# Kernel optimization log

Hardware: AMD Instinct MI355X
Metric: run time of the kernel (lower is better)

Reference implementation:

```python
import jax, jax.numpy as jnp
import numpy as np

N = 50000
E = 800000
DIN = 128
DH = [128, 128]
DOUT = 64


def setup_inputs() -> dict:
    key = jax.random.key(0)
    ks = jax.random.split(key, 12)

    def w(k, fan_in, fan_out):
        return jax.random.normal(k, (fan_in, fan_out), dtype=jnp.float32) / np.sqrt(fan_in)

    x = jax.random.normal(ks[0], (N, DIN), dtype=jnp.float32)
    edge_index = jax.random.randint(ks[1], (2, E), 0, N, dtype=jnp.int64)
    return {
        "x": x,
        "edge_index": edge_index,
        # SAGEConv layer 0: lin_l (aggregated neighbors, with bias), lin_r (root, no bias)
        "Wl0": w(ks[2], DIN, DH[0]), "Wr0": w(ks[3], DIN, DH[0]), "b0": jnp.zeros((DH[0],), jnp.float32),
        # SAGEConv layer 1
        "Wl1": w(ks[4], DH[0], DH[1]), "Wr1": w(ks[5], DH[0], DH[1]), "b1": jnp.zeros((DH[1],), jnp.float32),
        # final Linear
        "Wout": w(ks[6], DH[1], DOUT), "bout": jnp.zeros((DOUT,), jnp.float32),
    }


def sage_conv(h, src, dst, Wl, Wr, b):
    # mean-aggregate source features at destination nodes
    msg = h[src]                                                  # [E, d]
    agg = jax.ops.segment_sum(msg, dst, num_segments=N)           # [N, d]
    cnt = jax.ops.segment_sum(jnp.ones((src.shape[0],), h.dtype), dst, num_segments=N)
    agg = agg / jnp.maximum(cnt, 1.0)[:, None]
    return agg @ Wl + h @ Wr + b


def reference(x, edge_index, Wl0, Wr0, b0, Wl1, Wr1, b1, Wout, bout):
    src, dst = edge_index[0], edge_index[1]
    h = jax.nn.relu(sage_conv(x, src, dst, Wl0, Wr0, b0))
    # dropout: identity in eval mode
    h = jax.nn.relu(sage_conv(h, src, dst, Wl1, Wr1, b1))
    out = h @ Wout + bout                                         # [N, DOUT]
    return jax.nn.softmax(out, axis=1)
```

## Files before the change

kernel.cpp:

```cpp
#include <hip/hip_runtime.h>


#define CAP 64
#define NBK 256
#define EPB 2048
#define BCAP8 768
#define ASTR 136

typedef __attribute__((ext_vector_type(8))) short bf16x8;
typedef __attribute__((ext_vector_type(4))) float f32x4;

__device__ __forceinline__ unsigned short bf16_rtne(float f) {
    unsigned u = __float_as_uint(f);
    u += 0x7FFFu + ((u >> 16) & 1u);
    return (unsigned short)(u >> 16);
}

__device__ __forceinline__ unsigned pack2(float lo, float hi) {
    return (unsigned)bf16_rtne(lo) | ((unsigned)bf16_rtne(hi) << 16);
}

__device__ __forceinline__ void pack_w_body(const float* __restrict__ Wl,
                                            const float* __restrict__ Wr,
                                            unsigned short* __restrict__ Wp, int i) {
    int j = i & 7;
    int l = (i >> 3) & 63;
    int ntile = (i >> 9) & 7;
    int kstep = i >> 12;
    int k = kstep * 32 + (l >> 4) * 8 + j;
    int n = ntile * 16 + (l & 15);
    float v = (k < 128) ? Wl[k * 128 + n] : Wr[(k - 128) * 128 + n];
    Wp[i] = bf16_rtne(v);
}

__global__ __launch_bounds__(256) void bucket_prep_kernel(
        const int* __restrict__ src, const int* __restrict__ dst,
        unsigned int* __restrict__ gtail, unsigned int* __restrict__ gbuf,
        int E, int aBlocks,
        const float* __restrict__ x, unsigned short* __restrict__ xb, int n4, int cvtBlocks,
        const float* __restrict__ Wl0, const float* __restrict__ Wr0,
        unsigned short* __restrict__ Wp1,
        const float* __restrict__ Wl1, const float* __restrict__ Wr1,
        unsigned short* __restrict__ Wp2,
        const float* __restrict__ Wout, unsigned short* __restrict__ Wpo) {
    int b = blockIdx.x;
    if (b < aBlocks) {
        __shared__ unsigned int hist[NBK];
        __shared__ unsigned int pref[NBK + 1];
        __shared__ int baseS[NBK];
        __shared__ unsigned int scat[EPB];
        __shared__ unsigned char scatb[EPB];
        int tid = (int)threadIdx.x;
        int xcd = b & 7;
        hist[tid] = 0u;
        __syncthreads();

        int e0 = b * EPB + tid * 8;
        int dd[8], ss[8], bb[8];
        unsigned rr[8];
        bool vld[8];
        if (e0 + 7 < E) {
            int4 d0 = *(const int4*)(dst + e0);
            int4 d1 = *(const int4*)(dst + e0 + 4);
            int4 s0 = *(const int4*)(src + e0);
            int4 s1 = *(const int4*)(src + e0 + 4);
            dd[0] = d0.x; dd[1] = d0.y; dd[2] = d0.z; dd[3] = d0.w;
            dd[4] = d1.x; dd[5] = d1.y; dd[6] = d1.z; dd[7] = d1.w;
            ss[0] = s0.x; ss[1] = s0.y; ss[2] = s0.z; ss[3] = s0.w;
            ss[4] = s1.x; ss[5] = s1.y; ss[6] = s1.z; ss[7] = s1.w;
#pragma unroll
            for (int u = 0; u < 8; ++u) vld[u] = true;
        } else {
#pragma unroll
            for (int u = 0; u < 8; ++u) {
                int e = e0 + u;
                vld[u] = (e < E);
                dd[u] = vld[u] ? dst[e] : 0;
                ss[u] = vld[u] ? src[e] : 0;
            }
        }
#pragma unroll
        for (int u = 0; u < 8; ++u) {
            bb[u] = dd[u] >> 8;
            rr[u] = vld[u] ? atomicAdd(&hist[bb[u]], 1u) : 0u;
        }
        __syncthreads();
        pref[tid + 1] = hist[tid];
        if (tid == 0) pref[0] = 0u;
        __syncthreads();
        for (int off = 1; off < NBK; off <<= 1) {
            unsigned add = (tid + 1 > off) ? pref[tid + 1 - off] : 0u;
            __syncthreads();
            pref[tid + 1] += add;
            __syncthreads();
        }
        {
            unsigned h = hist[tid];
            unsigned gb0 = (h != 0u) ? atomicAdd(&gtail[xcd * NBK + tid], h) : 0u;
            baseS[tid] = (int)((unsigned)(xcd * NBK + tid) * BCAP8 + gb0) - (int)pref[tid];
        }
        __syncthreads();
#pragma unroll
        for (int u = 0; u < 8; ++u) {
            if (vld[u]) {
                unsigned idx = pref[bb[u]] + rr[u];
                scat[idx] = ((unsigned)dd[u] << 16) | (unsigned)(ss[u] & 0xFFFF);
                scatb[idx] = (unsigned char)bb[u];
            }
        }
        __syncthreads();
        unsigned tot = pref[NBK];
        for (unsigned i = (unsigned)tid; i < tot; i += 256u) {
            int bk = (int)scatb[i];
            int gi = baseS[bk] + (int)i;
            unsigned segBase = (unsigned)(xcd * NBK + bk) * BCAP8;
            if ((unsigned)gi - segBase < BCAP8) gbuf[gi] = scat[i];
        }
    } else if (b < aBlocks + cvtBlocks) {
        int i = (b - aBlocks) * 256 + (int)threadIdx.x;
        if (i < n4) {
            float4 v = ((const float4*)x)[i];
            ushort4 o;
            o.x = bf16_rtne(v.x); o.y = bf16_rtne(v.y);
            o.z = bf16_rtne(v.z); o.w = bf16_rtne(v.w);
            ((ushort4*)xb)[i] = o;
        }
    } else if (b < aBlocks + cvtBlocks + 128) {
        pack_w_body(Wl0, Wr0, Wp1, (b - aBlocks - cvtBlocks) * 256 + (int)threadIdx.x);
    } else if (b < aBlocks + cvtBlocks + 256) {
        pack_w_body(Wl1, Wr1, Wp2, (b - aBlocks - cvtBlocks - 128) * 256 + (int)threadIdx.x);
    } else {
        int i = (b - aBlocks - cvtBlocks - 256) * 256 + (int)threadIdx.x;
        int j = i & 7;
        int l = (i >> 3) & 63;
        int nt = (i >> 9) & 3;
        int ks = i >> 11;
        int k = ks * 32 + (l >> 4) * 8 + j;
        int n = nt * 16 + (l & 15);
        Wpo[i] = bf16_rtne(Wout[k * 64 + n]);
    }
}

__global__ __launch_bounds__(256) void fill_csr_kernel(
        const unsigned int* __restrict__ gtail, const unsigned int* __restrict__ gbuf,
        int* __restrict__ cnt, unsigned short* __restrict__ csr, int N) {
    __shared__ unsigned int cntL[256];
    __shared__ unsigned short stage[256 * CAP];
    int b = blockIdx.x;
    int tid = (int)threadIdx.x;
    cntL[tid] = 0u;
    __syncthreads();
#pragma unroll 1
    for (int xcd = 0; xcd < 8; ++xcd) {
        unsigned nE = gtail[xcd * NBK + b];
        if (nE > BCAP8) nE = BCAP8;
        const unsigned int* g = gbuf + (size_t)(xcd * NBK + b) * BCAP8;
        for (unsigned i = (unsigned)tid; i < nE; i += 256u) {
            unsigned pk = g[i];
            int dl = (int)((pk >> 16) & 255u);
            unsigned p = atomicAdd(&cntL[dl], 1u);
            if (p < CAP) stage[dl * CAP + p] = (unsigned short)(pk & 0xFFFFu);
        }
    }
    __syncthreads();
    const uint4* s4 = (const uint4*)stage;
    uint4* g4 = (uint4*)(csr + (size_t)b * (256 * CAP));
    for (int i = tid; i < (256 * CAP) / 8; i += 256) g4[i] = s4[i];
    int node = b * 256 + tid;
    if (node < N) cnt[node] = (int)cntL[tid];
}

__device__ __forceinline__ void gather_mean_lds(
        const unsigned* __restrict__ hu,
        const int* __restrict__ cnt,
        const unsigned short* __restrict__ csr, unsigned short* __restrict__ sAw,
        int m0, int lane, int N) {
    int qw = lane >> 4;
    int ql = lane & 15;
    int degs[4], bases[4];
#pragma unroll
    for (int i = 0; i < 4; ++i) {
        int node = m0 + qw * 4 + i;
        degs[i] = (node < N) ? min(cnt[node], CAP) : 0;
        bases[i] = node * CAP;
    }
#pragma unroll 1
    for (int s = 0; s < 4; ++s) {
#pragma unroll 1
        for (int i = 0; i < 4; ++i) {
            int nl = qw * 4 + i;
            int deg = degs[i];
            int s0 = bases[i];
            int s1 = s0 + deg;
            float a0 = 0.f, a1 = 0.f;
            for (int base = 0; base < deg; base += 16) {
                int nc = min(16, deg - base);
                int e = min(s0 + base + ql, s1 - 1);
                int idx = csr[e];
                for (int j = 0; j < nc; j += 8) {
                    unsigned v[8];
#pragma unroll
                    for (int u = 0; u < 8; ++u) {
                        int sidx = __shfl(idx, j + u, 16);
                        v[u] = hu[(size_t)sidx * 64 + s * 16 + ql];
                    }
#pragma unroll
                    for (int u = 0; u < 8; ++u) {
                        unsigned w = (j + u < nc) ? v[u] : 0u;
                        a0 += __uint_as_float(w << 16);
                        a1 += __uint_as_float(w & 0xFFFF0000u);
                    }
                }
            }
            float inv = 1.0f / (float)max(deg, 1);
            *(unsigned*)(sAw + nl * ASTR + s * 32 + ql * 2) = pack2(a0 * inv, a1 * inv);
        }
    }
}

__device__ __forceinline__ void mfma_dual_gemm_lds(
        const unsigned short* __restrict__ sAw, const unsigned short* __restrict__ rootb,
        const unsigned short* __restrict__ Wp, int rowc, int quad, int c, int lane,
        f32x4 acc[8]) {
#pragma unroll
    for (int t = 0; t < 8; ++t) acc[t] = (f32x4){0.f, 0.f, 0.f, 0.f};
    for (int ks = 0; ks < 8; ++ks) {
        bf16x8 a;
        if (ks < 4) a = *(const bf16x8*)(sAw + c * ASTR + ks * 32 + quad * 8);
        else        a = *(const bf16x8*)(rootb + (size_t)rowc * 128 + (ks & 3) * 32 + quad * 8);
#pragma unroll
        for (int t = 0; t < 8; ++t) {
            bf16x8 bf = *(const bf16x8*)(Wp + ((size_t)(ks * 8 + t) * 64 + lane) * 8);
            acc[t] = __builtin_amdgcn_mfma_f32_16x16x32_bf16(a, bf, acc[t], 0, 0, 0);
        }
    }
}

__global__ __launch_bounds__(256) void fused_l1_kernel(
        const unsigned short* __restrict__ hb, const int* __restrict__ cnt,
        const unsigned short* __restrict__ csr, const unsigned short* __restrict__ Wp,
        const float* __restrict__ b, unsigned short* __restrict__ houtb, int N) {
    __shared__ unsigned short sA[4][16 * ASTR];
    int lane = threadIdx.x & 63;
    int wv = threadIdx.x >> 6;
    int m0 = blockIdx.x * 64 + wv * 16;
    gather_mean_lds((const unsigned*)hb, cnt, csr, &sA[wv][0], m0, lane, N);
    int quad = lane >> 4;
    int c = lane & 15;
    int rowc = min(m0 + c, N - 1);
    f32x4 acc[8];
    mfma_dual_gemm_lds(&sA[wv][0], hb, Wp, rowc, quad, c, lane, acc);
#pragma unroll
    for (int t = 0; t < 8; ++t) {
        int col = t * 16 + c;
        float bias = b[col];
#pragma unroll
        for (int r = 0; r < 4; ++r) {
            sA[wv][(quad * 4 + r) * ASTR + col] = bf16_rtne(fmaxf(acc[t][r] + bias, 0.f));
        }
    }
    {
        int qw = lane >> 4, ql = lane & 15;
#pragma unroll
        for (int i = 0; i < 4; ++i) {
            int nl = qw * 4 + i;
            int node = m0 + nl;
            if (node < N) {
                uint4 row = *(const uint4*)(&sA[wv][nl * ASTR + ql * 8]);
                *(uint4*)(houtb + (size_t)node * 128 + ql * 8) = row;
            }
        }
    }
}

__global__ __launch_bounds__(256) void fused_l2_kernel(
        const unsigned short* __restrict__ hb, const int* __restrict__ cnt,
        const unsigned short* __restrict__ csr, const unsigned short* __restrict__ Wp,
        const float* __restrict__ b,
        const unsigned short* __restrict__ Wpo, const float* __restrict__ bout,
        float* __restrict__ out, int N) {
    __shared__ unsigned short sA[4][16 * ASTR];
    int lane = threadIdx.x & 63;
    int wv = threadIdx.x >> 6;
    int m0 = blockIdx.x * 64 + wv * 16;
    gather_mean_lds((const unsigned*)hb, cnt, csr, &sA[wv][0], m0, lane, N);
    int quad = lane >> 4;
    int c = lane & 15;
    int rowc = min(m0 + c, N - 1);
    f32x4 acc[8];
    mfma_dual_gemm_lds(&sA[wv][0], hb, Wp, rowc, quad, c, lane, acc);
#pragma unroll
    for (int t = 0; t < 8; ++t) {
        int col = t * 16 + c;
        float bias = b[col];
#pragma unroll
        for (int r = 0; r < 4; ++r) {
            sA[wv][(quad * 4 + r) * ASTR + col] = bf16_rtne(fmaxf(acc[t][r] + bias, 0.f));
        }
    }

    f32x4 acc2[4];
#pragma unroll
    for (int nt = 0; nt < 4; ++nt) acc2[nt] = (f32x4){0.f, 0.f, 0.f, 0.f};
#pragma unroll
    for (int ks = 0; ks < 4; ++ks) {
        bf16x8 a = *(const bf16x8*)&sA[wv][c * ASTR + ks * 32 + quad * 8];
#pragma unroll
        for (int nt = 0; nt < 4; ++nt) {
            bf16x8 bf = *(const bf16x8*)(Wpo + ((size_t)(ks * 4 + nt) * 64 + lane) * 8);
            acc2[nt] = __builtin_amdgcn_mfma_f32_16x16x32_bf16(a, bf, acc2[nt], 0, 0, 0);
        }
    }

    float bo[4];
#pragma unroll
    for (int nt = 0; nt < 4; ++nt) bo[nt] = bout[nt * 16 + c];
#pragma unroll
    for (int r = 0; r < 4; ++r) {
        float v[4];
#pragma unroll
        for (int nt = 0; nt < 4; ++nt) v[nt] = acc2[nt][r] + bo[nt];
        float m = fmaxf(fmaxf(v[0], v[1]), fmaxf(v[2], v[3]));
#pragma unroll
        for (int ofs = 1; ofs < 16; ofs <<= 1) m = fmaxf(m, __shfl_xor(m, ofs, 64));
        float e[4];
        float s = 0.f;
#pragma unroll
        for (int nt = 0; nt < 4; ++nt) { e[nt] = __expf(v[nt] - m); s += e[nt]; }
#pragma unroll
        for (int ofs = 1; ofs < 16; ofs <<= 1) s += __shfl_xor(s, ofs, 64);
        float inv = 1.0f / s;
        int node = m0 + quad * 4 + r;
        if (node < N) {
#pragma unroll
            for (int nt = 0; nt < 4; ++nt)
                out[(size_t)node * 64 + nt * 16 + c] = e[nt] * inv;
        }
    }
}

extern "C" void kernel_launch(void* const* d_in, const int* in_sizes, int n_in,
                              void* d_out, int out_size, void* d_ws, size_t ws_size,
                              hipStream_t stream) {
    const float* x    = (const float*)d_in[0];
    const int*   ei   = (const int*)d_in[1];
    const float* Wl0  = (const float*)d_in[2];
    const float* Wr0  = (const float*)d_in[3];
    const float* b0   = (const float*)d_in[4];
    const float* Wl1  = (const float*)d_in[5];
    const float* Wr1  = (const float*)d_in[6];
    const float* b1   = (const float*)d_in[7];
    const float* Wout = (const float*)d_in[8];
    const float* bout = (const float*)d_in[9];

    int N = in_sizes[0] / 128;
    int E = in_sizes[1] / 2;
    const int* src = ei;
    const int* dst = ei + E;
    int nb = (N + 255) >> 8;

    char* p = (char*)d_ws;
    auto alloc = [&](size_t bytes) -> char* {
        char* r = p;
        p += (bytes + 255) & ~(size_t)255;
        return r;
    };
    unsigned int*   gtail = (unsigned int*)alloc((size_t)8 * NBK * 4);
    unsigned int*   gbuf  = (unsigned int*)alloc((size_t)8 * NBK * BCAP8 * 4);
    int*            cnt   = (int*)alloc((size_t)N * 4);
    unsigned short* csr   = (unsigned short*)alloc((size_t)nb * 256 * CAP * 2);
    unsigned short* xb    = (unsigned short*)alloc((size_t)N * 128 * 2);
    unsigned short* h0b   = (unsigned short*)alloc((size_t)N * 128 * 2);
    unsigned short* Wp1   = (unsigned short*)alloc((size_t)32768 * 2);
    unsigned short* Wp2   = (unsigned short*)alloc((size_t)32768 * 2);
    unsigned short* Wpo   = (unsigned short*)alloc((size_t)8192 * 2);

    hipMemsetAsync(gtail, 0, (size_t)8 * NBK * 4, stream);

    int n4 = N * 128 / 4;
    int cvtBlocks = (n4 + 255) / 256;
    int aBlocks = (E + EPB - 1) / EPB;
    bucket_prep_kernel<<<aBlocks + cvtBlocks + 256 + 32, 256, 0, stream>>>(
        src, dst, gtail, gbuf, E, aBlocks,
        x, xb, n4, cvtBlocks, Wl0, Wr0, Wp1, Wl1, Wr1, Wp2, Wout, Wpo);

    fill_csr_kernel<<<nb, 256, 0, stream>>>(gtail, gbuf, cnt, csr, N);

    int gb = (N + 63) / 64;
    fused_l1_kernel<<<gb, 256, 0, stream>>>(xb, cnt, csr, Wp1, b0, h0b, N);
    fused_l2_kernel<<<gb, 256, 0, stream>>>(h0b, cnt, csr, Wp2, b1,
                                            Wpo, bout, (float*)d_out, N);
}
```

Measured before the change: 225.6 us.

## Sort CSR neighbors by source range and gather full rows per lane

The CSR fill now does a two-pass counting sort. Each node's neighbor list is grouped into four source-index ranges, and the per-range counts are packed into one 32-bit word. The gather loop walks those ranges in order, so all waves in flight touch a similar quarter of the feature table, which is meant to improve L2 locality. Each lane also loads a full 16-byte chunk per neighbor and accumulates 8 values per node, rather than making four passes of 4-byte loads. In exchange the fill kernel reads the edge buffer twice, the gather holds more live registers (a 4x8 accumulator array), and per-range counts saturate at 255.

```diff
diff --git a/kernel.cpp b/kernel.cpp
--- a/kernel.cpp
+++ b/kernel.cpp
@@ -6,6 +6,8 @@
 #define EPB 2048
 #define BCAP8 768
 #define ASTR 136
+#define NR 4
+#define RSH 14
 
 typedef __attribute__((ext_vector_type(8))) short bf16x8;
 typedef __attribute__((ext_vector_type(4))) float f32x4;
@@ -143,12 +145,14 @@
 
 __global__ __launch_bounds__(256) void fill_csr_kernel(
         const unsigned int* __restrict__ gtail, const unsigned int* __restrict__ gbuf,
-        int* __restrict__ cnt, unsigned short* __restrict__ csr, int N) {
-    __shared__ unsigned int cntL[256];
+        unsigned int* __restrict__ cnt4, unsigned short* __restrict__ csr, int N) {
+    __shared__ unsigned int cntR[256 * NR];
+    __shared__ unsigned int offR[256 * NR];
     __shared__ unsigned short stage[256 * CAP];
     int b = blockIdx.x;
     int tid = (int)threadIdx.x;
-    cntL[tid] = 0u;
+#pragma unroll
+    for (int r = 0; r < NR; ++r) cntR[r * 256 + tid] = 0u;
     __syncthreads();
 #pragma unroll 1
     for (int xcd = 0; xcd < 8; ++xcd) {
@@ -158,7 +162,36 @@
         for (unsigned i = (unsigned)tid; i < nE; i += 256u) {
             unsigned pk = g[i];
             int dl = (int)((pk >> 16) & 255u);
-            unsigned p = atomicAdd(&cntL[dl], 1u);
+            int rg = (int)((pk & 0xFFFFu) >> RSH);
+            atomicAdd(&cntR[dl * NR + rg], 1u);
+        }
+    }
+    __syncthreads();
+    {
+        unsigned c0 = cntR[tid * NR + 0], c1 = cntR[tid * NR + 1];
+        unsigned c2 = cntR[tid * NR + 2], c3 = cntR[tid * NR + 3];
+        offR[tid * NR + 0] = 0u;
+        offR[tid * NR + 1] = c0;
+        offR[tid * NR + 2] = c0 + c1;
+        offR[tid * NR + 3] = c0 + c1 + c2;
+        int node = b * 256 + tid;
+        if (node < N)
+            cnt4[node] = min(c0, 255u) | (min(c1, 255u) << 8) |
+                         (min(c2, 255u) << 16) | (min(c3, 255u) << 24);
+        cntR[tid * NR + 0] = 0u; cntR[tid * NR + 1] = 0u;
+        cntR[tid * NR + 2] = 0u; cntR[tid * NR + 3] = 0u;
+    }
+    __syncthreads();
+#pragma unroll 1
+    for (int xcd = 0; xcd < 8; ++xcd) {
+        unsigned nE = gtail[xcd * NBK + b];
+        if (nE > BCAP8) nE = BCAP8;
+        const unsigned int* g = gbuf + (size_t)(xcd * NBK + b) * BCAP8;
+        for (unsigned i = (unsigned)tid; i < nE; i += 256u) {
+            unsigned pk = g[i];
+            int dl = (int)((pk >> 16) & 255u);
+            int rg = (int)((pk & 0xFFFFu) >> RSH);
+            unsigned p = atomicAdd(&cntR[dl * NR + rg], 1u) + offR[dl * NR + rg];
             if (p < CAP) stage[dl * CAP + p] = (unsigned short)(pk & 0xFFFFu);
         }
     }
@@ -166,55 +199,89 @@
     const uint4* s4 = (const uint4*)stage;
     uint4* g4 = (uint4*)(csr + (size_t)b * (256 * CAP));
     for (int i = tid; i < (256 * CAP) / 8; i += 256) g4[i] = s4[i];
-    int node = b * 256 + tid;
-    if (node < N) cnt[node] = (int)cntL[tid];
 }
 
 __device__ __forceinline__ void gather_mean_lds(
-        const unsigned* __restrict__ hu,
-        const int* __restrict__ cnt,
+        const uint4* __restrict__ h4,
+        const unsigned* __restrict__ cnt4,
         const unsigned short* __restrict__ csr, unsigned short* __restrict__ sAw,
         int m0, int lane, int N) {
     int qw = lane >> 4;
     int ql = lane & 15;
-    int degs[4], bases[4];
+    float a[4][8];
+#pragma unroll
+    for (int i = 0; i < 4; ++i)
+#pragma unroll
+        for (int u = 0; u < 8; ++u) a[i][u] = 0.f;
+    unsigned pc[4];
+    int s0[4];
 #pragma unroll
     for (int i = 0; i < 4; ++i) {
         int node = m0 + qw * 4 + i;
-        degs[i] = (node < N) ? min(cnt[node], CAP) : 0;
-        bases[i] = node * CAP;
+        pc[i] = (node < N) ? cnt4[node] : 0u;
+        s0[i] = node * CAP;
     }
 #pragma unroll 1
-    for (int s = 0; s < 4; ++s) {
+    for (int r = 0; r < NR; ++r) {
+#pragma unroll
+        for (int i = 0; i < 4; ++i) {
+            unsigned c = pc[i];
+            int prefv = 0;
+#pragma unroll
+            for (int q = 0; q < NR; ++q)
+                if (q < r) prefv += (int)((c >> (8 * q)) & 255u);
+            int cr = (int)((c >> (8 * r)) & 255u);
+            int st = min(prefv, CAP);
+            int en = min(prefv + cr, CAP);
+            int base0 = s0[i];
 #pragma unroll 1
-        for (int i = 0; i < 4; ++i) {
-            int nl = qw * 4 + i;
-            int deg = degs[i];
-            int s0 = bases[i];
-            int s1 = s0 + deg;
-            float a0 = 0.f, a1 = 0.f;
-            for (int base = 0; base < deg; base += 16) {
-                int nc = min(16, deg - base);
-                int e = min(s0 + base + ql, s1 - 1);
+            for (int base = st; base < en; base += 16) {
+                int nc = min(en - base, 16);
+                int e = min(base0 + base + ql, base0 + en - 1);
                 int idx = csr[e];
+#pragma unroll 1
                 for (int j = 0; j < nc; j += 8) {
-                    unsigned v[8];
+                    uint4 v[8];
+                    bool ok[8];
 #pragma unroll
                     for (int u = 0; u < 8; ++u) {
-                        int sidx = __shfl(idx, j + u, 16);
-                        v[u] = hu[(size_t)sidx * 64 + s * 16 + ql];
+                        ok[u] = (j + u < nc);
+                        if (ok[u]) {
+                            int sidx = __shfl(idx, j + u, 16);
+                            v[u] = h4[(size_t)sidx * 16 + ql];
+                        }
                     }
 #pragma unroll
                     for (int u = 0; u < 8; ++u) {
-                        unsigned w = (j + u < nc) ? v[u] : 0u;
-                        a0 += __uint_as_float(w << 16);
-                        a1 += __uint_as_float(w & 0xFFFF0000u);
+                        if (ok[u]) {
+                            a[i][0] += __uint_as_float(v[u].x << 16);
+                            a[i][1] += __uint_as_float(v[u].x & 0xFFFF0000u);
+                            a[i][2] += __uint_as_float(v[u].y << 16);
+                            a[i][3] += __uint_as_float(v[u].y & 0xFFFF0000u);
+                            a[i][4] += __uint_as_float(v[u].z << 16);
+                            a[i][5] += __uint_as_float(v[u].z & 0xFFFF0000u);
+                            a[i][6] += __uint_as_float(v[u].w << 16);
+                            a[i][7] += __uint_as_float(v[u].w & 0xFFFF0000u);
+                        }
                     }
                 }
             }
-            float inv = 1.0f / (float)max(deg, 1);
-            *(unsigned*)(sAw + nl * ASTR + s * 32 + ql * 2) = pack2(a0 * inv, a1 * inv);
-        }
+        }
+    }
+#pragma unroll
+    for (int i = 0; i < 4; ++i) {
+        unsigned c = pc[i];
+        int tot = (int)((c & 255u) + ((c >> 8) & 255u) +
+                        ((c >> 16) & 255u) + ((c >> 24) & 255u));
+        int deg = min(tot, CAP);
+        float inv = 1.0f / (float)max(deg, 1);
+        int nl = qw * 4 + i;
+        uint4 o;
+        o.x = pack2(a[i][0] * inv, a[i][1] * inv);
+        o.y = pack2(a[i][2] * inv, a[i][3] * inv);
+        o.z = pack2(a[i][4] * inv, a[i][5] * inv);
+        o.w = pack2(a[i][6] * inv, a[i][7] * inv);
+        *(uint4*)(sAw + nl * ASTR + ql * 8) = o;
     }
 }
 
@@ -237,14 +304,14 @@
 }
 
 __global__ __launch_bounds__(256) void fused_l1_kernel(
-        const unsigned short* __restrict__ hb, const int* __restrict__ cnt,
+        const unsigned short* __restrict__ hb, const unsigned* __restrict__ cnt4,
         const unsigned short* __restrict__ csr, const unsigned short* __restrict__ Wp,
         const float* __restrict__ b, unsigned short* __restrict__ houtb, int N) {
     __shared__ unsigned short sA[4][16 * ASTR];
     int lane = threadIdx.x & 63;
     int wv = threadIdx.x >> 6;
     int m0 = blockIdx.x * 64 + wv * 16;
-    gather_mean_lds((const unsigned*)hb, cnt, csr, &sA[wv][0], m0, lane, N);
+    gather_mean_lds((const uint4*)hb, cnt4, csr, &sA[wv][0], m0, lane, N);
     int quad = lane >> 4;
     int c = lane & 15;
     int rowc = min(m0 + c, N - 1);
@@ -274,7 +341,7 @@
 }
 
 __global__ __launch_bounds__(256) void fused_l2_kernel(
-        const unsigned short* __restrict__ hb, const int* __restrict__ cnt,
+        const unsigned short* __restrict__ hb, const unsigned* __restrict__ cnt4,
         const unsigned short* __restrict__ csr, const unsigned short* __restrict__ Wp,
         const float* __restrict__ b,
         const unsigned short* __restrict__ Wpo, const float* __restrict__ bout,
@@ -283,7 +350,7 @@
     int lane = threadIdx.x & 63;
     int wv = threadIdx.x >> 6;
     int m0 = blockIdx.x * 64 + wv * 16;
-    gather_mean_lds((const unsigned*)hb, cnt, csr, &sA[wv][0], m0, lane, N);
+    gather_mean_lds((const uint4*)hb, cnt4, csr, &sA[wv][0], m0, lane, N);
     int quad = lane >> 4;
     int c = lane & 15;
     int rowc = min(m0 + c, N - 1);
@@ -367,7 +434,7 @@
     };
     unsigned int*   gtail = (unsigned int*)alloc((size_t)8 * NBK * 4);
     unsigned int*   gbuf  = (unsigned int*)alloc((size_t)8 * NBK * BCAP8 * 4);
-    int*            cnt   = (int*)alloc((size_t)N * 4);
+    unsigned int*   cnt4  = (unsigned int*)alloc((size_t)N * 4);
     unsigned short* csr   = (unsigned short*)alloc((size_t)nb * 256 * CAP * 2);
     unsigned short* xb    = (unsigned short*)alloc((size_t)N * 128 * 2);
     unsigned short* h0b   = (unsigned short*)alloc((size_t)N * 128 * 2);
@@ -384,10 +451,10 @@
         src, dst, gtail, gbuf, E, aBlocks,
         x, xb, n4, cvtBlocks, Wl0, Wr0, Wp1, Wl1, Wr1, Wp2, Wout, Wpo);
 
-    fill_csr_kernel<<<nb, 256, 0, stream>>>(gtail, gbuf, cnt, csr, N);
+    fill_csr_kernel<<<nb, 256, 0, stream>>>(gtail, gbuf, cnt4, csr, N);
 
     int gb = (N + 63) / 64;
-    fused_l1_kernel<<<gb, 256, 0, stream>>>(xb, cnt, csr, Wp1, b0, h0b, N);
-    fused_l2_kernel<<<gb, 256, 0, stream>>>(h0b, cnt, csr, Wp2, b1,
+    fused_l1_kernel<<<gb, 256, 0, stream>>>(xb, cnt4, csr, Wp1, b0, h0b, N);
+    fused_l2_kernel<<<gb, 256, 0, stream>>>(h0b, cnt4, csr, Wp2, b1,
                                             Wpo, bout, (float*)d_out, N);
 }
```

Result: slower. 300.7 us (+33.3%).
